# Performance work log

Measured on AMD Instinct MI355X. Metric: run time of the kernel, lower is better.

## Reference

```python
import jax, jax.numpy as jnp
import numpy as np

N, B, D, K_IN, P = 64, 256, 1792, 35, 10
EPS = 1e-5


def setup_inputs() -> dict:
    key = jax.random.key(0)
    ks = jax.random.split(key, 8)
    s_tok = 1.0 / np.sqrt(K_IN)
    s_net = 1.0 / np.sqrt(D)
    return {
        "X": jax.random.normal(ks[0], (N, B, D), dtype=jnp.float32),
        "task_id": jax.random.normal(ks[1], (B, K_IN), dtype=jnp.float32),
        # tokens: Linear(35, 10*1792)
        "W_tok": jax.random.uniform(ks[2], (P * D, K_IN), jnp.float32, -s_tok, s_tok),
        "b_tok": jax.random.uniform(ks[3], (P * D,), jnp.float32, -s_tok, s_tok),
        # ptokens: Linear(35, 1792)
        "W_ptok": jax.random.uniform(ks[4], (D, K_IN), jnp.float32, -s_tok, s_tok),
        "b_ptok": jax.random.uniform(ks[5], (D,), jnp.float32, -s_tok, s_tok),
        # LayerNorm(1792)
        "gamma": jnp.ones((D,), jnp.float32),
        "beta": jnp.zeros((D,), jnp.float32),
        # net: Linear(1792, 10)
        "W_net": jax.random.uniform(ks[6], (P, D), jnp.float32, -s_net, s_net),
        "b_net": jax.random.uniform(ks[7], (P,), jnp.float32, -s_net, s_net),
    }


def _layernorm(x, gamma, beta):
    mu = jnp.mean(x, axis=-1, keepdims=True)
    var = jnp.mean(jnp.square(x - mu), axis=-1, keepdims=True)
    return (x - mu) * jax.lax.rsqrt(var + EPS) * gamma + beta


def reference(X, task_id, W_tok, b_tok, W_ptok, b_ptok, gamma, beta, W_net, b_net):
    # ptokens(task_id): (b, D); identical across n, so compute once and broadcast.
    ptok = task_id @ W_ptok.T + b_ptok                       # (b, D)
    task_token = _layernorm(ptok[None, :, :] + X, gamma, beta)  # (n, b, D)
    # net -> sigmoid: per-token mixing weights over P prompts.
    weight = jax.nn.sigmoid(task_token @ W_net.T + b_net)    # (n, b, P)
    # tokens(task_id): (b, P, D); identical across n, broadcast in einsum.
    prompt_bank = (task_id @ W_tok.T + b_tok).reshape(B, P, D)  # (b, P, D)
    prompt = jnp.einsum("nbp,bpd->nbd", weight, prompt_bank)  # (n, b, D)
    return X + prompt
```

## Files before the change

kernel.cpp:

```cpp
#include <hip/hip_runtime.h>
#include <hip/hip_bf16.h>

#define NN 64
#define BB 256
#define DD 1792
#define KK 35
#define PP 10
#define DQ 448
#define GR 8
#define NGRP 28

__device__ __forceinline__ float group16_sum_dpp(float x) {
    asm("v_add_f32_dpp %0, %0, %0 row_shr:1 row_mask:0xf bank_mask:0xf bound_ctrl:0" : "+v"(x));
    asm("v_add_f32_dpp %0, %0, %0 row_shr:2 row_mask:0xf bank_mask:0xf bound_ctrl:0" : "+v"(x));
    asm("v_add_f32_dpp %0, %0, %0 row_shr:4 row_mask:0xf bank_mask:0xf bound_ctrl:0" : "+v"(x));
    asm("v_add_f32_dpp %0, %0, %0 row_shr:8 row_mask:0xf bank_mask:0xf bound_ctrl:0" : "+v"(x));
    return x;
}

__global__ void prep_gf(const float* __restrict__ gamma, const float* __restrict__ beta,
                        const float* __restrict__ Wnet, const float* __restrict__ bnet,
                        float* __restrict__ GF, float* __restrict__ SG, float* __restrict__ ZC) {
    const int p = blockIdx.x;
    const int tid = threadIdx.x;
    float sg = 0.f, sb = 0.f;
#pragma unroll
    for (int j = 0; j < 7; ++j) {
        int d = j * 256 + tid;
        float wv = Wnet[p * DD + d];
        float g = gamma[d] * wv;
        GF[p * DD + d] = g;
        sg += g;
        sb += beta[d] * wv;
    }
#pragma unroll
    for (int off = 32; off > 0; off >>= 1) {
        sg += __shfl_xor(sg, off);
        sb += __shfl_xor(sb, off);
    }
    __shared__ float rs[4][2];
    if ((tid & 63) == 0) { rs[tid >> 6][0] = sg; rs[tid >> 6][1] = sb; }
    __syncthreads();
    if (tid == 0) {
        float a = 0.f, c = 0.f;
#pragma unroll
        for (int w = 0; w < 4; ++w) { a += rs[w][0]; c += rs[w][1]; }
        SG[p] = a;
        ZC[p] = c + bnet[p];
    }
}

__global__ void prep_bank(const float* __restrict__ task,
                          const float* __restrict__ Wtok, const float* __restrict__ btok,
                          const float* __restrict__ Wptok, const float* __restrict__ bptok,
                          float* __restrict__ bank, float* __restrict__ ptok) {
    __shared__ float ti[32 * KK];
    const int tid = threadIdx.x;
    const int b0 = blockIdx.y * 32;
    for (int i = tid; i < 32 * KK; i += 256) ti[i] = task[b0 * KK + i];

    const int r = blockIdx.x * 256 + tid;
    const bool isbank = (r < PP * DD);
    const int rr = isbank ? r : (r - PP * DD);
    const float* __restrict__ W = isbank ? Wtok : Wptok;
    const float bias = isbank ? btok[r] : bptok[rr];

    float w[KK];
#pragma unroll
    for (int k = 0; k < KK; ++k) w[k] = W[rr * KK + k];

    __syncthreads();
#pragma unroll 1
    for (int bb = 0; bb < 32; ++bb) {
        float acc = bias;
#pragma unroll
        for (int k = 0; k < KK; ++k) acc = fmaf(ti[bb * KK + k], w[k], acc);
        const int b = b0 + bb;
        if (isbank) bank[b * (PP * DD) + r] = acc;
        else        ptok[b * DD + rr]       = acc;
    }
}

__global__ __launch_bounds__(448, 1) void fused_pipe(
    const float* __restrict__ X, const float* __restrict__ BANK,
    const float* __restrict__ PTOK, const float* __restrict__ GF,
    const float* __restrict__ SG, const float* __restrict__ ZC,
    float* __restrict__ OUT) {
    const int tid = threadIdx.x;
    const int b = blockIdx.x;

    const float4* __restrict__ X4 = (const float4*)X;
    const float4* __restrict__ B4 = (const float4*)BANK;
    const float4* __restrict__ G4 = (const float4*)GF;
    const float4* __restrict__ P4 = (const float4*)PTOK;
    float4* __restrict__ O4 = (float4*)OUT;

    __shared__ float red[2][GR][NGRP][12];
    __shared__ float wlds[2][GR][PP];

    const float4 ptk = P4[(size_t)b * DQ + tid];
    float4 gf[PP];
#pragma unroll
    for (int p = 0; p < PP; ++p) gf[p] = G4[(size_t)p * DQ + tid];
    float4 bk[PP];
#pragma unroll
    for (int p = 0; p < PP; ++p) bk[p] = B4[((size_t)b * PP + p) * DQ + tid];

    const bool writer = ((tid & 15) == 15);
    const int g16 = tid >> 4;

    float4 x0[GR], x1[GR], x2[GR];

#define BURST(XN, GN)                                                              \
    {                                                                              \
        _Pragma("unroll")                                                          \
        for (int r = 0; r < GR; ++r)                                               \
            XN[r] = X4[((size_t)((GN) * GR + r) * BB + b) * DQ + tid];             \
        __builtin_amdgcn_sched_barrier(0);                                         \
    }

#define BARRIER_RAW()                                                              \
    asm volatile("s_waitcnt lgkmcnt(0)" ::: "memory");                             \
    __builtin_amdgcn_sched_barrier(0);                                             \
    __builtin_amdgcn_s_barrier();                                                  \
    __builtin_amdgcn_sched_barrier(0);

#define PHASE1(XC, RB)                                                             \
    {                                                                              \
        _Pragma("unroll")                                                          \
        for (int r = 0; r < GR; ++r) {                                             \
            float4 t;                                                              \
            t.x = XC[r].x + ptk.x; t.y = XC[r].y + ptk.y;                          \
            t.z = XC[r].z + ptk.z; t.w = XC[r].w + ptk.w;                          \
            float s1 = t.x + t.y + t.z + t.w;                                      \
            float s2 = t.x * t.x;                                                  \
            s2 = fmaf(t.y, t.y, s2); s2 = fmaf(t.z, t.z, s2);                      \
            s2 = fmaf(t.w, t.w, s2);                                               \
            float a[PP];                                                           \
            _Pragma("unroll")                                                      \
            for (int p = 0; p < PP; ++p) {                                         \
                float v = t.x * gf[p].x;                                           \
                v = fmaf(t.y, gf[p].y, v);                                         \
                v = fmaf(t.z, gf[p].z, v);                                         \
                v = fmaf(t.w, gf[p].w, v);                                         \
                a[p] = v;                                                          \
            }                                                                      \
            s1 = group16_sum_dpp(s1);                                              \
            s2 = group16_sum_dpp(s2);                                              \
            _Pragma("unroll")                                                      \
            for (int p = 0; p < PP; ++p) a[p] = group16_sum_dpp(a[p]);             \
            if (writer) {                                                          \
                float4* dst = (float4*)&red[RB][r][g16][0];                        \
                dst[0] = make_float4(s1, s2, a[0], a[1]);                          \
                dst[1] = make_float4(a[2], a[3], a[4], a[5]);                      \
                dst[2] = make_float4(a[6], a[7], a[8], a[9]);                      \
            }                                                                      \
        }                                                                          \
    }

#define FINALIZE(RB)                                                               \
    if (tid < GR * 16) {                                                           \
        const int row = tid >> 4;                                                  \
        const int v = tid & 15;                                                    \
        float f = 0.f;                                                             \
        if (v < 12) {                                                              \
            _Pragma("unroll")                                                      \
            for (int q = 0; q < NGRP; ++q) f += red[RB][row][q][v];                \
        }                                                                          \
        const int bse = (tid & 63) & ~15;                                          \
        const float mu = __shfl(f, bse)     * (1.0f / (float)DD);                  \
        const float ms = __shfl(f, bse + 1) * (1.0f / (float)DD);                  \
        const float istd = rsqrtf(ms - mu * mu + 1e-5f);                           \
        if (v >= 2 && v < 12) {                                                    \
            const int p = v - 2;                                                   \
            const float z = istd * (f - mu * SG[p]) + ZC[p];                       \
            wlds[RB][row][p] = 1.0f / (1.0f + __expf(-z));                         \
        }                                                                          \
    }

#define PHASE2(XC, WB, GN)                                                         \
    {                                                                              \
        _Pragma("unroll")                                                          \
        for (int r = 0; r < GR; ++r) {                                             \
            float4 acc = XC[r];                                                    \
            _Pragma("unroll")                                                      \
            for (int p = 0; p < PP; ++p) {                                         \
                const float wv = wlds[WB][r][p];                                   \
                acc.x = fmaf(wv, bk[p].x, acc.x);                                  \
                acc.y = fmaf(wv, bk[p].y, acc.y);                                  \
                acc.z = fmaf(wv, bk[p].z, acc.z);                                  \
                acc.w = fmaf(wv, bk[p].w, acc.w);                                  \
            }                                                                      \
            O4[((size_t)((GN) * GR + r) * BB + b) * DQ + tid] = acc;               \
        }                                                                          \
    }

    BURST(x0, 0)

    BURST(x1, 1) PHASE1(x0, 0) BARRIER_RAW() FINALIZE(0)
    BURST(x2, 2) PHASE1(x1, 1) BARRIER_RAW() FINALIZE(1) PHASE2(x0, 0, 0)
    BURST(x0, 3) PHASE1(x2, 0) BARRIER_RAW() FINALIZE(0) PHASE2(x1, 1, 1)
    BURST(x1, 4) PHASE1(x0, 1) BARRIER_RAW() FINALIZE(1) PHASE2(x2, 0, 2)
    BURST(x2, 5) PHASE1(x1, 0) BARRIER_RAW() FINALIZE(0) PHASE2(x0, 1, 3)
    BURST(x0, 6) PHASE1(x2, 1) BARRIER_RAW() FINALIZE(1) PHASE2(x1, 0, 4)
    BURST(x1, 7) PHASE1(x0, 0) BARRIER_RAW() FINALIZE(0) PHASE2(x2, 1, 5)
    PHASE1(x1, 1) BARRIER_RAW() FINALIZE(1) PHASE2(x0, 0, 6)
    BARRIER_RAW() PHASE2(x1, 1, 7)

#undef PHASE2
#undef FINALIZE
#undef PHASE1
#undef BARRIER_RAW
#undef BURST
}

extern "C" void kernel_launch(void* const* d_in, const int* in_sizes, int n_in,
                              void* d_out, int out_size, void* d_ws, size_t ws_size,
                              hipStream_t stream) {
    const float* X     = (const float*)d_in[0];
    const float* task  = (const float*)d_in[1];
    const float* Wtok  = (const float*)d_in[2];
    const float* btok  = (const float*)d_in[3];
    const float* Wptok = (const float*)d_in[4];
    const float* bptok = (const float*)d_in[5];
    const float* gamma = (const float*)d_in[6];
    const float* beta  = (const float*)d_in[7];
    const float* Wnet  = (const float*)d_in[8];
    const float* bnet  = (const float*)d_in[9];
    float* out = (float*)d_out;

    float* ws = (float*)d_ws;
    float* bank = ws;
    float* ptok = bank + (size_t)BB * PP * DD;
    float* GF   = ptok + (size_t)BB * DD;
    float* SG   = GF + PP * DD;
    float* ZC   = SG + PP;

    prep_gf<<<PP, 256, 0, stream>>>(gamma, beta, Wnet, bnet, GF, SG, ZC);
    prep_bank<<<dim3(77, 8), 256, 0, stream>>>(task, Wtok, btok, Wptok, bptok, bank, ptok);
    fused_pipe<<<BB, 448, 0, stream>>>(X, bank, ptok, GF, SG, ZC, out);
}
```

Measured before the change: 77.19 us.

## Split fused pipeline across two blocks per batch with rotated group order

Doubles the grid so each batch index is handled by two blocks, each covering half of the n-groups (4 groups of 8 rows instead of 8). The group order is rotated by batch index to spread concurrent memory accesses, and launch_bounds no longer forces one block per CU. Output stores become nontemporal to avoid polluting cache. The aim is better CU occupancy and latency hiding across 256 CUs. The cost is that each block reloads the bank and GF registers, and the pipeline is shorter, so more of it is prologue and epilogue.

```diff
diff --git a/kernel.cpp b/kernel.cpp
--- a/kernel.cpp
+++ b/kernel.cpp
@@ -10,6 +10,8 @@
 #define GR 8
 #define NGRP 28
 
+typedef float fx4 __attribute__((ext_vector_type(4)));
+
 __device__ __forceinline__ float group16_sum_dpp(float x) {
     asm("v_add_f32_dpp %0, %0, %0 row_shr:1 row_mask:0xf bank_mask:0xf bound_ctrl:0" : "+v"(x));
     asm("v_add_f32_dpp %0, %0, %0 row_shr:2 row_mask:0xf bank_mask:0xf bound_ctrl:0" : "+v"(x));
@@ -81,19 +83,26 @@
     }
 }
 
-__global__ __launch_bounds__(448, 1) void fused_pipe(
+__global__ __launch_bounds__(448) void fused_pipe(
     const float* __restrict__ X, const float* __restrict__ BANK,
     const float* __restrict__ PTOK, const float* __restrict__ GF,
     const float* __restrict__ SG, const float* __restrict__ ZC,
     float* __restrict__ OUT) {
-    const int tid = threadIdx.x;
-    const int b = blockIdx.x;
+    const int tid  = threadIdx.x;
+    const int b    = blockIdx.x & (BB - 1);
+    const int half = blockIdx.x >> 8;
+    const int rot  = b & 3;
+
+    const int G0 = half * 4 + ((0 + rot) & 3);
+    const int G1 = half * 4 + ((1 + rot) & 3);
+    const int G2 = half * 4 + ((2 + rot) & 3);
+    const int G3 = half * 4 + ((3 + rot) & 3);
 
     const float4* __restrict__ X4 = (const float4*)X;
     const float4* __restrict__ B4 = (const float4*)BANK;
     const float4* __restrict__ G4 = (const float4*)GF;
     const float4* __restrict__ P4 = (const float4*)PTOK;
-    float4* __restrict__ O4 = (float4*)OUT;
+    fx4* __restrict__ OO = (fx4*)OUT;
 
     __shared__ float red[2][GR][NGRP][12];
     __shared__ float wlds[2][GR][PP];
@@ -191,21 +200,19 @@
                 acc.z = fmaf(wv, bk[p].z, acc.z);                                  \
                 acc.w = fmaf(wv, bk[p].w, acc.w);                                  \
             }                                                                      \
-            O4[((size_t)((GN) * GR + r) * BB + b) * DQ + tid] = acc;               \
-        }                                                                          \
-    }
-
-    BURST(x0, 0)
-
-    BURST(x1, 1) PHASE1(x0, 0) BARRIER_RAW() FINALIZE(0)
-    BURST(x2, 2) PHASE1(x1, 1) BARRIER_RAW() FINALIZE(1) PHASE2(x0, 0, 0)
-    BURST(x0, 3) PHASE1(x2, 0) BARRIER_RAW() FINALIZE(0) PHASE2(x1, 1, 1)
-    BURST(x1, 4) PHASE1(x0, 1) BARRIER_RAW() FINALIZE(1) PHASE2(x2, 0, 2)
-    BURST(x2, 5) PHASE1(x1, 0) BARRIER_RAW() FINALIZE(0) PHASE2(x0, 1, 3)
-    BURST(x0, 6) PHASE1(x2, 1) BARRIER_RAW() FINALIZE(1) PHASE2(x1, 0, 4)
-    BURST(x1, 7) PHASE1(x0, 0) BARRIER_RAW() FINALIZE(0) PHASE2(x2, 1, 5)
-    PHASE1(x1, 1) BARRIER_RAW() FINALIZE(1) PHASE2(x0, 0, 6)
-    BARRIER_RAW() PHASE2(x1, 1, 7)
+            fx4 av; av.x = acc.x; av.y = acc.y; av.z = acc.z; av.w = acc.w;        \
+            __builtin_nontemporal_store(av,                                        \
+                &OO[((size_t)((GN) * GR + r) * BB + b) * DQ + tid]);               \
+        }                                                                          \
+    }
+
+    BURST(x0, G0)
+
+    BURST(x1, G1) PHASE1(x0, 0) BARRIER_RAW() FINALIZE(0)
+    BURST(x2, G2) PHASE1(x1, 1) BARRIER_RAW() FINALIZE(1) PHASE2(x0, 0, G0)
+    BURST(x0, G3) PHASE1(x2, 0) BARRIER_RAW() FINALIZE(0) PHASE2(x1, 1, G1)
+    PHASE1(x0, 1) BARRIER_RAW() FINALIZE(1) PHASE2(x2, 0, G2)
+    BARRIER_RAW() PHASE2(x0, 1, G3)
 
 #undef PHASE2
 #undef FINALIZE
@@ -238,5 +245,5 @@
 
     prep_gf<<<PP, 256, 0, stream>>>(gamma, beta, Wnet, bnet, GF, SG, ZC);
     prep_bank<<<dim3(77, 8), 256, 0, stream>>>(task, Wtok, btok, Wptok, bptok, bank, ptok);
-    fused_pipe<<<BB, 448, 0, stream>>>(X, bank, ptok, GF, SG, ZC, out);
-}
+    fused_pipe<<<2 * BB, 448, 0, stream>>>(X, bank, ptok, GF, SG, ZC, out);
+}
```

Measured after the change: 80.03 us. 1.04x slower.
